# Performance work log

Hardware: AMD Instinct MI355X
Metric: run time of the kernel (lower is better)

## Reference

```python
import jax, jax.numpy as jnp
import numpy as np


def _find(parent, x):
    # chase parent pointers to the root (root = min-rank node of its component)
    return jax.lax.while_loop(lambda v: parent[v] != v, lambda v: parent[v], x)


def _pd0_single(fcol, src, dst):
    """0-dim persistence diagram for one filtration column.

    Semantics match TOGL.generate_persistence_diagram_dim0:
      - nodes are added in sorted order of fcol; birth(node) = its sorted rank
      - directed edge (u, v) merges components at step rank(v) iff rank(u) < rank(v)
      - elder rule: the component whose root has the larger rank dies
      - output row i = (birth=i, death) for the node of rank i (insertion order of
        the original dict is exactly rank order); death = inf for survivors.
    """
    n = fcol.shape[0]
    order = jnp.argsort(fcol)
    rank = jnp.zeros((n,), jnp.int32).at[order].set(jnp.arange(n, dtype=jnp.int32))
    a = rank[src]                      # rank-space endpoints
    b = rank[dst]
    valid = a < b                      # only edges whose source is already active fire
    w = jnp.where(valid, b, n)         # edge weight = step at which it fires
    perm = jnp.argsort(w)              # Kruskal order
    ea, eb, ev = a[perm], b[perm], valid[perm]

    def step(carry, e):
        parent, deaths = carry
        ia, ib, v = e
        ra = _find(parent, ia)
        rb = _find(parent, ib)
        merge = v & (ra != rb)
        elder = jnp.minimum(ra, rb)
        younger = jnp.maximum(ra, rb)
        deaths = deaths.at[younger].set(jnp.where(merge, ib.astype(deaths.dtype), deaths[younger]))
        parent = parent.at[younger].set(jnp.where(merge, elder, parent[younger]))
        # path compression at the two queried nodes
        parent = parent.at[ia].set(jnp.where(merge, elder, ra))
        parent = parent.at[ib].set(jnp.where(merge, elder, rb))
        return (parent, deaths), None

    parent0 = jnp.arange(n, dtype=jnp.int32)
    deaths0 = jnp.full((n,), jnp.inf, jnp.float32)
    (parent, deaths), _ = jax.lax.scan(step, (parent0, deaths0), (ea, eb, ev))
    births = jnp.arange(n, dtype=jnp.float32)
    return jnp.stack([births, deaths], axis=1)  # (n_nodes, 2)


def setup_inputs() -> dict:
    key = jax.random.key(0)
    k = jax.random.split(key, 6)
    N, F, H, NF, E = 20000, 1024, 2048, 4, 160000
    X = jax.random.normal(k[0], (N, F), jnp.float32)
    edge_index = jax.random.randint(k[1], (2, E), 0, N, jnp.int64)
    W1 = jax.random.normal(k[2], (F, H), jnp.float32) / np.sqrt(F)
    b1 = jax.random.normal(k[3], (H,), jnp.float32) * 0.01
    W2 = jax.random.normal(k[4], (H, NF), jnp.float32) / np.sqrt(H)
    b2 = jax.random.normal(k[5], (NF,), jnp.float32) * 0.01
    return {"X": X, "edge_index": edge_index, "W1": W1, "b1": b1, "W2": W2, "b2": b2}


def reference(X, edge_index, W1, b1, W2, b2):
    # filter_graph: Linear -> ReLU -> Linear
    filt = jnp.maximum(X @ W1 + b1, 0.0) @ W2 + b2            # (N, n_filtrations)
    src = edge_index[0].astype(jnp.int32)
    dst = edge_index[1].astype(jnp.int32)
    diagrams = jax.vmap(_pd0_single, in_axes=(1, None, None))(filt, src, dst)  # (NF, N, 2)
    return filt, diagrams
```

## Files before the change

kernel.cpp:

```cpp
#include <hip/hip_runtime.h>

typedef unsigned long long u64;
typedef unsigned int u32;
typedef unsigned short ushort_t;
typedef __attribute__((ext_vector_type(8))) short short8;
typedef __attribute__((ext_vector_type(4))) float fx4;

#define F_DIM 1024
#define H_DIM 2048
#define NFOUT 4
#define WS_W1T_OFF (1u << 20)

__device__ __forceinline__ ushort_t f2bf(float x)
{
    union { float f; u32 u; } c; c.f = x;
    u32 b = c.u;
    u32 r = b + 0x7FFFu + ((b >> 16) & 1u);
    return (ushort_t)(r >> 16);
}
__device__ __forceinline__ float bf2f(ushort_t h)
{
    union { u32 u; float f; } c; c.u = ((u32)h) << 16;
    return c.f;
}
__device__ __forceinline__ void split3(float x, ushort_t& u0, ushort_t& u1, ushort_t& u2)
{
    u0 = f2bf(x);
    float r1 = x - bf2f(u0);
    u1 = f2bf(r1);
    float r2 = r1 - bf2f(u1);
    u2 = f2bf(r2);
}

__global__ __launch_bounds__(256)
void k_w1split(const float* __restrict__ W1, ushort_t* __restrict__ w1t)
{
    __shared__ __align__(16) ushort_t LT[3][64][72];
    const int t = threadIdx.x;
    const int bk = blockIdx.x >> 5;
    const int bh = blockIdx.x & 31;
    const int k0 = bk * 64, h0 = bh * 64;
    const int kk = t >> 4, hb = (t & 15) * 4;
    #pragma unroll
    for (int j = 0; j < 4; j++) {
        int row = kk + j * 16;
        float4 v = *(const float4*)(W1 + (size_t)(k0 + row) * H_DIM + h0 + hb);
        float xs[4] = { v.x, v.y, v.z, v.w };
        #pragma unroll
        for (int c = 0; c < 4; c++) {
            ushort_t u0, u1, u2;
            split3(xs[c], u0, u1, u2);
            LT[0][hb + c][row] = u0;
            LT[1][hb + c][row] = u1;
            LT[2][hb + c][row] = u2;
        }
    }
    __syncthreads();
    const int hl = t >> 2, sg = t & 3;
    #pragma unroll
    for (int p = 0; p < 3; p++)
        #pragma unroll
        for (int q = 0; q < 2; q++) {
            int ks = sg * 16 + q * 8;
            *(short8*)(w1t + (size_t)p * (H_DIM * (size_t)F_DIM)
                       + (size_t)(h0 + hl) * F_DIM + k0 + ks) =
                *(const short8*)&LT[p][hl][ks];
        }
}

__device__ __forceinline__ fx4 mfma16(short8 a, short8 b, fx4 c)
{
    return __builtin_amdgcn_mfma_f32_16x16x32_bf16(a, b, c, 0, 0, 0);
}

#define AP_BYTES (3 * 128 * 128)
#define BP_BYTES (3 * 256 * 128)
#define W2_OFF   (AP_BYTES + BP_BYTES)
#define SM_BYTES (W2_OFF + 256 * 4 * 4)
#define HPITCH 260

__global__ __launch_bounds__(512, 2)
void k_filt_mfma(const float* __restrict__ X, const ushort_t* __restrict__ w1t,
                 const float* __restrict__ b1, const float* __restrict__ W2,
                 const float* __restrict__ b2, float* __restrict__ out, int N)
{
    extern __shared__ char smem[];
    char* Ac = smem;
    char* Bc = smem + AP_BYTES;
    float* W2s = (float*)(smem + W2_OFF);
    float* hid = (float*)smem;

    const int t = threadIdx.x;
    const int lane = t & 63;
    const int w = t >> 6;
    const int wr = (w >> 2) * 64;
    const int wc = (w & 3) * 64;
    const int r0 = blockIdx.x * 128;
    const int l15 = lane & 15, l4 = lane >> 4;
    const int fsw = (l15 & 7) << 4;

    const int arow = t >> 2;
    const int aq   = (t & 3);
    const bool arow_ok = (r0 + arow) < N;
    const int brow = t >> 1;
    const int bseg = (t & 1) * 64;

    const int orow = t >> 2;
    const int onf  = t & 3;

    float Afl[16];
    short8 Bv[12];
    fx4 acc[4][4];
    float pacc = 0.f;
    #pragma unroll
    for (int i = 0; i < 4; i++)
        #pragma unroll
        for (int j = 0; j < 4; j++) acc[i][j] = (fx4)(0.f);

    {
        if (arow_ok) {
            #pragma unroll
            for (int q = 0; q < 4; q++) {
                float4 v = *(const float4*)(X + (size_t)(r0 + arow) * F_DIM + aq * 16 + q * 4);
                Afl[q * 4 + 0] = v.x; Afl[q * 4 + 1] = v.y;
                Afl[q * 4 + 2] = v.z; Afl[q * 4 + 3] = v.w;
            }
        } else {
            #pragma unroll
            for (int j = 0; j < 16; j++) Afl[j] = 0.f;
        }
        #pragma unroll
        for (int p = 0; p < 3; p++)
            #pragma unroll
            for (int q = 0; q < 4; q++)
                Bv[p * 4 + q] = *(const short8*)(w1t + (size_t)p * (H_DIM * (size_t)F_DIM)
                                 + (size_t)brow * F_DIM + bseg / 2 + q * 8);
    }

    for (int it = 0; it < 128; ++it) {
        const int hc = it >> 4, kc = it & 15;

        ushort_t s0[16], s1[16], s2[16];
        #pragma unroll
        for (int j = 0; j < 16; j++) split3(Afl[j], s0[j], s1[j], s2[j]);

        __syncthreads();

        {
            const int aswz = (arow & 7) << 4;
            #pragma unroll
            for (int p = 0; p < 3; p++) {
                const ushort_t* sp = (p == 0) ? s0 : (p == 1) ? s1 : s2;
                #pragma unroll
                for (int h = 0; h < 2; h++) {
                    short8 pk;
                    #pragma unroll
                    for (int i = 0; i < 8; i++) pk[i] = (short)sp[h * 8 + i];
                    *(short8*)(Ac + p * 16384 + arow * 128 + ((aq * 32 + h * 16) ^ aswz)) = pk;
                }
            }
            const int bswz = (brow & 7) << 4;
            #pragma unroll
            for (int p = 0; p < 3; p++)
                #pragma unroll
                for (int q = 0; q < 4; q++)
                    *(short8*)(Bc + p * 32768 + brow * 128 + ((bseg + q * 16) ^ bswz)) = Bv[p * 4 + q];
            if (kc == 0 && t < 256)
                *(float4*)&W2s[t * 4] = *(const float4*)(W2 + ((size_t)hc * 256 + t) * NFOUT);
        }

        if (it + 1 < 128) {
            const int hn = (it + 1) >> 4, kn = (it + 1) & 15;
            if (arow_ok) {
                #pragma unroll
                for (int q = 0; q < 4; q++) {
                    float4 v = *(const float4*)(X + (size_t)(r0 + arow) * F_DIM + kn * 64 + aq * 16 + q * 4);
                    Afl[q * 4 + 0] = v.x; Afl[q * 4 + 1] = v.y;
                    Afl[q * 4 + 2] = v.z; Afl[q * 4 + 3] = v.w;
                }
            }
            #pragma unroll
            for (int p = 0; p < 3; p++)
                #pragma unroll
                for (int q = 0; q < 4; q++)
                    Bv[p * 4 + q] = *(const short8*)(w1t + (size_t)p * (H_DIM * (size_t)F_DIM)
                                     + (size_t)(hn * 256 + brow) * F_DIM + kn * 64 + bseg / 2 + q * 8);
        }

        __syncthreads();

        #pragma unroll
        for (int sub = 0; sub < 2; ++sub) {
            const int kb = sub * 64 + l4 * 16;
            short8 b[4][3];
            #pragma unroll
            for (int cf = 0; cf < 4; ++cf) {
                const int hrow = wc + cf * 16 + l15;
                #pragma unroll
                for (int p = 0; p < 3; p++)
                    b[cf][p] = *(const short8*)(Bc + p * 32768 + hrow * 128 + (kb ^ fsw));
            }
            #pragma unroll
            for (int rr = 0; rr < 4; ++rr) {
                const int row = wr + rr * 16 + l15;
                short8 a0 = *(const short8*)(Ac + 0 * 16384 + row * 128 + (kb ^ fsw));
                short8 a1 = *(const short8*)(Ac + 1 * 16384 + row * 128 + (kb ^ fsw));
                short8 a2 = *(const short8*)(Ac + 2 * 16384 + row * 128 + (kb ^ fsw));
                #pragma unroll
                for (int cf = 0; cf < 4; ++cf) {
                    fx4 c = acc[rr][cf];
                    c = mfma16(a0, b[cf][0], c);
                    c = mfma16(a0, b[cf][1], c);
                    c = mfma16(a1, b[cf][0], c);
                    c = mfma16(a0, b[cf][2], c);
                    c = mfma16(a1, b[cf][1], c);
                    c = mfma16(a2, b[cf][0], c);
                    acc[rr][cf] = c;
                }
            }
        }

        if (kc == 15) {
            __syncthreads();
            #pragma unroll
            for (int rr = 0; rr < 4; ++rr)
                #pragma unroll
                for (int cf = 0; cf < 4; ++cf) {
                    const int hl = wc + cf * 16 + l15;
                    const float bias1 = b1[hc * 256 + hl];
                    #pragma unroll
                    for (int g = 0; g < 4; g++) {
                        const int rl = wr + rr * 16 + l4 * 4 + g;
                        hid[rl * HPITCH + hl] = fmaxf(acc[rr][cf][g] + bias1, 0.f);
                    }
                    acc[rr][cf] = (fx4)(0.f);
                }
            __syncthreads();
            {
                const float* hp = hid + orow * HPITCH;
                #pragma unroll 16
                for (int j = 0; j < 256; j++)
                    pacc = fmaf(hp[j], W2s[j * 4 + onf], pacc);
            }
        }
    }

    {
        const int rg = r0 + orow;
        if (rg < N) out[(size_t)rg * NFOUT + onf] = pacc + b2[onf];
    }
}

#define BM 64
#define BH 64
#define KCH 64
#define LROW 68

__global__ __launch_bounds__(256, 2)
void k_filt(const float* __restrict__ X, const float* __restrict__ W1,
            const float* __restrict__ b1, const float* __restrict__ W2,
            const float* __restrict__ b2, float* __restrict__ out, int N)
{
    __shared__ float Xs[KCH * LROW];
    __shared__ float Ws[KCH * LROW];
    __shared__ float W2s[BH * NFOUT];
    const int t = threadIdx.x;
    const int r0 = blockIdx.x * BM;
    const int tr = t >> 4, tc = t & 15;
    const int orow = t >> 2, onf = t & 3;
    float fchain = 0.0f;
    for (int hc = 0; hc < H_DIM; hc += BH) {
        float acc[4][4];
        #pragma unroll
        for (int i = 0; i < 4; i++)
            #pragma unroll
            for (int j = 0; j < 4; j++) acc[i][j] = 0.0f;
        for (int kc = 0; kc < F_DIM; kc += KCH) {
            {
                const int rowq = t >> 4, kkq = t & 15;
                float xv[4][4];
                #pragma unroll
                for (int j = 0; j < 4; j++) {
                    int r = r0 + rowq * 4 + j;
                    float4 v = (r < N) ? *(const float4*)(X + (size_t)r * F_DIM + kc + kkq * 4)
                                       : make_float4(0.f, 0.f, 0.f, 0.f);
                    xv[j][0] = v.x; xv[j][1] = v.y; xv[j][2] = v.z; xv[j][3] = v.w;
                }
                #pragma unroll
                for (int j = 0; j < 4; j++)
                    *(float4*)&Xs[(kkq * 4 + j) * LROW + rowq * 4] =
                        make_float4(xv[0][j], xv[1][j], xv[2][j], xv[3][j]);
            }
            {
                const int hq = t & 15;
                #pragma unroll
                for (int q = 0; q < 4; q++) {
                    int kk = (t >> 4) + q * 16;
                    *(float4*)&Ws[kk * LROW + hq * 4] =
                        *(const float4*)(W1 + (size_t)(kc + kk) * H_DIM + hc + hq * 4);
                }
            }
            __syncthreads();
            #pragma unroll 8
            for (int kk = 0; kk < KCH; kk++) {
                float4 xv = *(float4*)&Xs[kk * LROW + tr * 4];
                float4 wv = *(float4*)&Ws[kk * LROW + tc * 4];
                acc[0][0] = fmaf(xv.x, wv.x, acc[0][0]); acc[0][1] = fmaf(xv.x, wv.y, acc[0][1]);
                acc[0][2] = fmaf(xv.x, wv.z, acc[0][2]); acc[0][3] = fmaf(xv.x, wv.w, acc[0][3]);
                acc[1][0] = fmaf(xv.y, wv.x, acc[1][0]); acc[1][1] = fmaf(xv.y, wv.y, acc[1][1]);
                acc[1][2] = fmaf(xv.y, wv.z, acc[1][2]); acc[1][3] = fmaf(xv.y, wv.w, acc[1][3]);
                acc[2][0] = fmaf(xv.z, wv.x, acc[2][0]); acc[2][1] = fmaf(xv.z, wv.y, acc[2][1]);
                acc[2][2] = fmaf(xv.z, wv.z, acc[2][2]); acc[2][3] = fmaf(xv.z, wv.w, acc[2][3]);
                acc[3][0] = fmaf(xv.w, wv.x, acc[3][0]); acc[3][1] = fmaf(xv.w, wv.y, acc[3][1]);
                acc[3][2] = fmaf(xv.w, wv.z, acc[3][2]); acc[3][3] = fmaf(xv.w, wv.w, acc[3][3]);
            }
            __syncthreads();
        }
        {
            float4 bv = *(const float4*)(b1 + hc + tc * 4);
            #pragma unroll
            for (int i = 0; i < 4; i++) {
                float4 hv;
                hv.x = fmaxf(acc[i][0] + bv.x, 0.f);
                hv.y = fmaxf(acc[i][1] + bv.y, 0.f);
                hv.z = fmaxf(acc[i][2] + bv.z, 0.f);
                hv.w = fmaxf(acc[i][3] + bv.w, 0.f);
                *(float4*)&Ws[(tr * 4 + i) * LROW + tc * 4] = hv;
            }
            if (t < BH)
                *(float4*)&W2s[t * 4] = *(const float4*)(W2 + (size_t)(hc + t) * NFOUT);
        }
        __syncthreads();
        #pragma unroll 16
        for (int hh = 0; hh < BH; hh++)
            fchain = fmaf(Ws[orow * LROW + hh], W2s[hh * 4 + onf], fchain);
        __syncthreads();
    }
    {
        int r = r0 + orow;
        if (r < N) out[(size_t)r * NFOUT + onf] = fchain + b2[onf];
    }
}

__global__ void k_prep(u32* __restrict__ rank, int N)
{
    int g = blockIdx.x * blockDim.x + threadIdx.x;
    if (g < 4 * N) rank[g] = 0u;
}

#define JTILE 2048

__global__ __launch_bounds__(256)
void k_rank(const float* __restrict__ filt, u32* __restrict__ rank,
            int N, int nchunk)
{
    __shared__ float4 lds[JTILE];
    const int chunk = blockIdx.x % nchunk;
    const int jslice = blockIdx.x / nchunk;
    const int jt = jslice * JTILE;
    const int i = chunk * 256 + threadIdx.x;
    const bool iok = i < N;
    float4 vi = iok ? *(const float4*)(filt + (size_t)i * 4)
                    : make_float4(0.f, 0.f, 0.f, 0.f);
    for (int s = 0; s < JTILE; s += 256) {
        int j = jt + s + threadIdx.x;
        lds[s + threadIdx.x] = (j < N)
            ? *(const float4*)(filt + (size_t)j * 4)
            : make_float4(INFINITY, INFINITY, INFINITY, INFINITY);
    }
    __syncthreads();
    int c0 = 0, c1 = 0, c2 = 0, c3 = 0;
    #pragma unroll 4
    for (int jj = 0; jj < JTILE; jj++) {
        float4 vj = lds[jj];
        int j = jt + jj;
        bool jlt = j < i;
        c0 += (vj.x < vi.x) || (vj.x == vi.x && jlt);
        c1 += (vj.y < vi.y) || (vj.y == vi.y && jlt);
        c2 += (vj.z < vi.z) || (vj.z == vi.z && jlt);
        c3 += (vj.w < vi.w) || (vj.w == vi.w && jlt);
    }
    if (iok) {
        atomicAdd(&rank[0 * N + i], (u32)c0);
        atomicAdd(&rank[1 * N + i], (u32)c1);
        atomicAdd(&rank[2 * N + i], (u32)c2);
        atomicAdd(&rank[3 * N + i], (u32)c3);
    }
}

__device__ __forceinline__ u32 lds_aload(u32* p)
{
    return __hip_atomic_load(p, __ATOMIC_RELAXED, __HIP_MEMORY_SCOPE_WORKGROUP);
}

__device__ __forceinline__ u32 rep_walk32(u32* S, u32 u, u32 t, u32& sv_out)
{
    u32 sv = lds_aload(&S[u]);
    while ((sv >> 16) <= t) {
        u = sv & 0xFFFFu;
        sv = lds_aload(&S[u]);
    }
    sv_out = sv;
    return u;
}

__device__ void do_merge32(u32* S, u32 u, u32 v, u32 t)
{
    for (int guard = 0; guard < (1 << 22); guard++) {
        u32 svu, svv;
        u = rep_walk32(S, u, t, svu);
        v = rep_walk32(S, v, t, svv);
        if (u == v) return;
        if (u < v) { u32 tm = u; u = v; v = tm; u32 ts = svu; svu = svv; svv = ts; }
        u32 s = svu >> 16;
        if (s <= t) continue;
        u32 des = (t << 16) | v;
        u32 old = atomicCAS(&S[u], svu, des);
        if (old == svu) {
            if (s == 0xFFFFu) return;
            u = v; v = old & 0xFFFFu;
            t = s;
        }
    }
}

__global__ __launch_bounds__(1024, 1)
void k_merge4(const int* __restrict__ eidx, const u32* __restrict__ rank,
              float* __restrict__ dg, int N, int E)
{
    extern __shared__ u32 S[];
    const int f = blockIdx.x;
    const u32* rk = rank + (size_t)f * N;

    for (int u = threadIdx.x; u < N; u += blockDim.x)
        S[u] = (0xFFFFu << 16) | (u32)u;
    __syncthreads();

    for (int e = threadIdx.x; e < E; e += blockDim.x) {
        u32 a = rk[eidx[e]];
        u32 b = rk[eidx[E + e]];
        if (a < b) do_merge32(S, a, b, b);
    }
    __syncthreads();

    for (int r = threadIdx.x; r < N; r += blockDim.x) {
        u32 s = S[r] >> 16;
        float death = (s == 0xFFFFu) ? 3.0e38f : (float)s;
        dg[(size_t)f * N * 2 + (size_t)r * 2 + 0] = (float)r;
        dg[(size_t)f * N * 2 + (size_t)r * 2 + 1] = death;
    }
}

extern "C" void kernel_launch(void* const* d_in, const int* in_sizes, int n_in,
                              void* d_out, int out_size, void* d_ws, size_t ws_size,
                              hipStream_t stream)
{
    const float* X  = (const float*)d_in[0];
    const int*   EI = (const int*)d_in[1];
    const float* W1 = (const float*)d_in[2];
    const float* b1 = (const float*)d_in[3];
    const float* W2 = (const float*)d_in[4];
    const float* b2 = (const float*)d_in[5];
    const int N = in_sizes[0] / F_DIM;
    const int E = in_sizes[1] / 2;

    float* out = (float*)d_out;
    float* dg  = out + (size_t)N * NFOUT;
    u32* rank  = (u32*)d_ws;

    static bool attr_set = false;
    if (!attr_set) {
        (void)hipFuncSetAttribute((const void*)k_merge4,
                                  hipFuncAttributeMaxDynamicSharedMemorySize,
                                  160 * 1024);
        (void)hipFuncSetAttribute((const void*)k_filt_mfma,
                                  hipFuncAttributeMaxDynamicSharedMemorySize,
                                  160 * 1024);
        attr_set = true;
    }

    k_prep<<<(4 * N + 255) / 256, 256, 0, stream>>>(rank, N);

    const size_t w1t_need = (size_t)WS_W1T_OFF + 3ull * H_DIM * F_DIM * 2;
    if (ws_size >= w1t_need) {
        ushort_t* w1t = (ushort_t*)((char*)d_ws + WS_W1T_OFF);
        k_w1split<<<512, 256, 0, stream>>>(W1, w1t);
        k_filt_mfma<<<(N + 127) / 128, 512, SM_BYTES, stream>>>(X, w1t, b1, W2, b2, out, N);
    } else {
        k_filt<<<(N + BM - 1) / BM, 256, 0, stream>>>(X, W1, b1, W2, b2, out, N);
    }

    const int nchunk = (N + 255) / 256;
    const int njt    = (N + JTILE - 1) / JTILE;
    k_rank<<<nchunk * njt, 256, 0, stream>>>(out, rank, N, nchunk);
    k_merge4<<<4, 1024, (size_t)N * sizeof(u32), stream>>>(EI, rank, dg, N, E);
}
```

Before: 1.603 ms.

## Pre-split X into bf16 planes and stream tiles directly into LDS

Adds a kernel that splits X once into three swizzled bf16 planes in workspace, and stores W1 pieces in the same swizzled layout. A new GEMM kernel loads A and B tiles straight into LDS with global_load_lds instead of splitting X per tile in registers. It also uses 80-row tiles so more blocks cover the CUs. In exchange it costs an extra pass over X with a large workspace write, runs at one block per CU, and has no double buffering, so load latency sits between the barriers.

Result: faster. 1.457 ms (-9.1%).

```diff
diff --git a/kernel.cpp b/kernel.cpp
--- a/kernel.cpp
+++ b/kernel.cpp
@@ -9,7 +9,9 @@
 #define F_DIM 1024
 #define H_DIM 2048
 #define NFOUT 4
-#define WS_W1T_OFF (1u << 20)
+#define WS_W1T_OFF (1ull << 20)
+#define WS_XS_OFF  (16ull << 20)
+#define PB_BYTES   ((size_t)H_DIM * F_DIM * 2)
 
 __device__ __forceinline__ ushort_t f2bf(float x)
 {
@@ -30,6 +32,13 @@
     u1 = f2bf(r1);
     float r2 = r1 - bf2f(u1);
     u2 = f2bf(r2);
+}
+
+__device__ __forceinline__ void gload16(const void* g, void* l)
+{
+    __builtin_amdgcn_global_load_lds(
+        (const __attribute__((address_space(1))) unsigned int*)g,
+        (__attribute__((address_space(3))) unsigned int*)l, 16, 0, 0);
 }
 
 __global__ __launch_bounds__(256)
@@ -57,20 +66,171 @@
     }
     __syncthreads();
     const int hl = t >> 2, sg = t & 3;
+    char* wb = (char*)w1t;
+    const int hsw = (hl & 7) << 4;
     #pragma unroll
     for (int p = 0; p < 3; p++)
         #pragma unroll
         for (int q = 0; q < 2; q++) {
             int ks = sg * 16 + q * 8;
-            *(short8*)(w1t + (size_t)p * (H_DIM * (size_t)F_DIM)
-                       + (size_t)(h0 + hl) * F_DIM + k0 + ks) =
+            *(short8*)(wb + (size_t)p * PB_BYTES + (size_t)(h0 + hl) * 2048
+                       + bk * 128 + ((ks * 2) ^ hsw)) =
                 *(const short8*)&LT[p][hl][ks];
         }
 }
 
+__global__ __launch_bounds__(256)
+void k_xsplit(const float* __restrict__ X, ushort_t* __restrict__ xs,
+              int N, int Npad)
+{
+    const int row = blockIdx.x;
+    if (row >= N) return;
+    const int t = threadIdx.x;
+    float4 v = *(const float4*)(X + (size_t)row * F_DIM + t * 4);
+    const int swz = (row & 7) << 4;
+    const int off = ((t * 8) & ~127) | (((t * 8) & 127) ^ swz);
+    const size_t PA = (size_t)Npad * 2048;
+    char* base = (char*)xs + (size_t)row * 2048 + off;
+    float in[4] = { v.x, v.y, v.z, v.w };
+    ushort4 u0, u1, u2;
+    ushort_t* p0 = (ushort_t*)&u0; ushort_t* p1 = (ushort_t*)&u1; ushort_t* p2 = (ushort_t*)&u2;
+    #pragma unroll
+    for (int j = 0; j < 4; j++) split3(in[j], p0[j], p1[j], p2[j]);
+    *(ushort4*)(base)          = u0;
+    *(ushort4*)(base + PA)     = u1;
+    *(ushort4*)(base + 2 * PA) = u2;
+}
+
 __device__ __forceinline__ fx4 mfma16(short8 a, short8 b, fx4 c)
 {
     return __builtin_amdgcn_mfma_f32_16x16x32_bf16(a, b, c, 0, 0, 0);
+}
+
+#define A4_BYTES (3 * 80 * 128)
+#define B4_BYTES (3 * 256 * 128)
+#define W24_OFF  (A4_BYTES + B4_BYTES)
+#define SM4_BYTES (W24_OFF + 256 * 4 * 4)
+#define HP4 260
+
+__global__ __launch_bounds__(512, 1)
+void k_filt_mfma4(const ushort_t* __restrict__ xs, const ushort_t* __restrict__ w1t,
+                  const float* __restrict__ b1, const float* __restrict__ W2,
+                  const float* __restrict__ b2, float* __restrict__ out,
+                  int N, int Npad)
+{
+    extern __shared__ char smem[];
+    char* Ac = smem;
+    char* Bc = smem + A4_BYTES;
+    float* W2s = (float*)(smem + W24_OFF);
+    float* hid = (float*)smem;
+
+    const int t = threadIdx.x;
+    const int lane = t & 63;
+    const int w = t >> 6;
+    const int wc = w * 32;
+    const int r0 = blockIdx.x * 80;
+    const int l15 = lane & 15, l4 = lane >> 4;
+    const int fsw = (l15 & 7) << 4;
+
+    const char* xsb = (const char*)xs;
+    const char* w1b = (const char*)w1t;
+    const size_t PA = (size_t)Npad * 2048;
+    const int laneoff = (lane >> 3) * 2048 + ((lane & 7) << 4);
+
+    const int orow = t >> 2;
+    const int onf  = t & 3;
+
+    fx4 acc[5][2];
+    #pragma unroll
+    for (int i = 0; i < 5; i++)
+        #pragma unroll
+        for (int j = 0; j < 2; j++) acc[i][j] = (fx4)(0.f);
+    float pacc = 0.f;
+
+    for (int it = 0; it < 128; ++it) {
+        const int hc = it >> 4, kc = it & 15;
+
+        __syncthreads();
+
+        for (int g = w; g < 126; g += 8) {
+            char* ldsb; const char* src;
+            if (g < 30) {
+                const int p = g / 10, rg = g - p * 10;
+                ldsb = Ac + p * 10240 + rg * 1024;
+                src  = xsb + (size_t)p * PA + (size_t)(r0 + rg * 8) * 2048 + kc * 128;
+            } else {
+                const int gb = g - 30;
+                const int p = gb >> 5, rg = gb & 31;
+                ldsb = Bc + p * 32768 + rg * 1024;
+                src  = w1b + (size_t)p * PB_BYTES + (size_t)(hc * 256 + rg * 8) * 2048 + kc * 128;
+            }
+            gload16(src + laneoff, ldsb);
+        }
+        if (kc == 0 && t < 256)
+            *(float4*)&W2s[t * 4] = *(const float4*)(W2 + ((size_t)hc * 256 + t) * NFOUT);
+
+        __syncthreads();
+
+        #pragma unroll
+        for (int sub = 0; sub < 2; ++sub) {
+            const int kb = (sub * 64 + l4 * 16) ^ fsw;
+            short8 b[2][3];
+            #pragma unroll
+            for (int cf = 0; cf < 2; ++cf) {
+                const int hrow = wc + cf * 16 + l15;
+                #pragma unroll
+                for (int p = 0; p < 3; p++)
+                    b[cf][p] = *(const short8*)(Bc + p * 32768 + hrow * 128 + kb);
+            }
+            #pragma unroll
+            for (int rr = 0; rr < 5; ++rr) {
+                const int row = rr * 16 + l15;
+                short8 a0 = *(const short8*)(Ac + 0 * 10240 + row * 128 + kb);
+                short8 a1 = *(const short8*)(Ac + 1 * 10240 + row * 128 + kb);
+                short8 a2 = *(const short8*)(Ac + 2 * 10240 + row * 128 + kb);
+                #pragma unroll
+                for (int cf = 0; cf < 2; ++cf) {
+                    fx4 c = acc[rr][cf];
+                    c = mfma16(a0, b[cf][0], c);
+                    c = mfma16(a0, b[cf][1], c);
+                    c = mfma16(a1, b[cf][0], c);
+                    c = mfma16(a0, b[cf][2], c);
+                    c = mfma16(a1, b[cf][1], c);
+                    c = mfma16(a2, b[cf][0], c);
+                    acc[rr][cf] = c;
+                }
+            }
+        }
+
+        if (kc == 15) {
+            __syncthreads();
+            #pragma unroll
+            for (int rr = 0; rr < 5; ++rr)
+                #pragma unroll
+                for (int cf = 0; cf < 2; ++cf) {
+                    const int hl = wc + cf * 16 + l15;
+                    const float bias1 = b1[hc * 256 + hl];
+                    #pragma unroll
+                    for (int g = 0; g < 4; g++) {
+                        const int rl = rr * 16 + l4 * 4 + g;
+                        hid[rl * HP4 + hl] = fmaxf(acc[rr][cf][g] + bias1, 0.f);
+                    }
+                    acc[rr][cf] = (fx4)(0.f);
+                }
+            __syncthreads();
+            if (orow < 80) {
+                const float* hp = hid + orow * HP4;
+                #pragma unroll 16
+                for (int j = 0; j < 256; j++)
+                    pacc = fmaf(hp[j], W2s[j * 4 + onf], pacc);
+            }
+        }
+    }
+
+    if (orow < 80) {
+        const int rg = r0 + orow;
+        if (rg < N) out[(size_t)rg * NFOUT + onf] = pacc + b2[onf];
+    }
 }
 
 #define AP_BYTES (3 * 128 * 128)
@@ -80,9 +240,9 @@
 #define HPITCH 260
 
 __global__ __launch_bounds__(512, 2)
-void k_filt_mfma(const float* __restrict__ X, const ushort_t* __restrict__ w1t,
-                 const float* __restrict__ b1, const float* __restrict__ W2,
-                 const float* __restrict__ b2, float* __restrict__ out, int N)
+void k_filt_mfma3(const float* __restrict__ X, const ushort_t* __restrict__ w1t,
+                  const float* __restrict__ b1, const float* __restrict__ W2,
+                  const float* __restrict__ b2, float* __restrict__ out, int N)
 {
     extern __shared__ char smem[];
     char* Ac = smem;
@@ -104,7 +264,6 @@
     const bool arow_ok = (r0 + arow) < N;
     const int brow = t >> 1;
     const int bseg = (t & 1) * 64;
-
     const int orow = t >> 2;
     const int onf  = t & 3;
 
@@ -133,8 +292,8 @@
         for (int p = 0; p < 3; p++)
             #pragma unroll
             for (int q = 0; q < 4; q++)
-                Bv[p * 4 + q] = *(const short8*)(w1t + (size_t)p * (H_DIM * (size_t)F_DIM)
-                                 + (size_t)brow * F_DIM + bseg / 2 + q * 8);
+                Bv[p * 4 + q] = *(const short8*)((const char*)w1t + (size_t)p * PB_BYTES
+                                 + (size_t)brow * 2048 + bseg + q * 16);
     }
 
     for (int it = 0; it < 128; ++it) {
@@ -183,8 +342,8 @@
             for (int p = 0; p < 3; p++)
                 #pragma unroll
                 for (int q = 0; q < 4; q++)
-                    Bv[p * 4 + q] = *(const short8*)(w1t + (size_t)p * (H_DIM * (size_t)F_DIM)
-                                     + (size_t)(hn * 256 + brow) * F_DIM + kn * 64 + bseg / 2 + q * 8);
+                    Bv[p * 4 + q] = *(const short8*)((const char*)w1t + (size_t)p * PB_BYTES
+                                     + (size_t)(hn * 256 + brow) * 2048 + kn * 128 + bseg + q * 16);
         }
 
         __syncthreads();
@@ -471,21 +630,30 @@
     static bool attr_set = false;
     if (!attr_set) {
         (void)hipFuncSetAttribute((const void*)k_merge4,
-                                  hipFuncAttributeMaxDynamicSharedMemorySize,
-                                  160 * 1024);
-        (void)hipFuncSetAttribute((const void*)k_filt_mfma,
-                                  hipFuncAttributeMaxDynamicSharedMemorySize,
-                                  160 * 1024);
+                                  hipFuncAttributeMaxDynamicSharedMemorySize, 160 * 1024);
+        (void)hipFuncSetAttribute((const void*)k_filt_mfma3,
+                                  hipFuncAttributeMaxDynamicSharedMemorySize, 160 * 1024);
+        (void)hipFuncSetAttribute((const void*)k_filt_mfma4,
+                                  hipFuncAttributeMaxDynamicSharedMemorySize, 160 * 1024);
         attr_set = true;
     }
 
     k_prep<<<(4 * N + 255) / 256, 256, 0, stream>>>(rank, N);
 
-    const size_t w1t_need = (size_t)WS_W1T_OFF + 3ull * H_DIM * F_DIM * 2;
-    if (ws_size >= w1t_need) {
+    const int Npad = ((N + 79) / 80) * 80;
+    const size_t need_w1t = WS_W1T_OFF + 3ull * PB_BYTES;
+    const size_t need_xs  = WS_XS_OFF + 3ull * (size_t)Npad * 2048;
+
+    if (ws_size >= need_xs) {
+        ushort_t* w1t = (ushort_t*)((char*)d_ws + WS_W1T_OFF);
+        ushort_t* xsp = (ushort_t*)((char*)d_ws + WS_XS_OFF);
+        k_w1split<<<512, 256, 0, stream>>>(W1, w1t);
+        k_xsplit<<<N, 256, 0, stream>>>(X, xsp, N, Npad);
+        k_filt_mfma4<<<Npad / 80, 512, SM4_BYTES, stream>>>(xsp, w1t, b1, W2, b2, out, N, Npad);
+    } else if (ws_size >= need_w1t) {
         ushort_t* w1t = (ushort_t*)((char*)d_ws + WS_W1T_OFF);
         k_w1split<<<512, 256, 0, stream>>>(W1, w1t);
-        k_filt_mfma<<<(N + 127) / 128, 512, SM_BYTES, stream>>>(X, w1t, b1, W2, b2, out, N);
+        k_filt_mfma3<<<(N + 127) / 128, 512, SM_BYTES, stream>>>(X, w1t, b1, W2, b2, out, N);
     } else {
         k_filt<<<(N + BM - 1) / BM, 256, 0, stream>>>(X, W1, b1, W2, b2, out, N);
     }
```
